# Kernel optimization log

Measured on AMD Instinct MI355X. Metric: run time of the kernel, lower is better.

The kernel has to match this reference:

```python
import jax, jax.numpy as jnp
import numpy as np

EPS = 1e-8


def setup_inputs() -> dict:
    key0 = jax.random.key(0)
    k1, k2, k3 = jax.random.split(key0, 3)
    B, Q, K, H, D = 8, 16, 65536, 1, 64
    query = jax.random.normal(k1, (B, Q, H, D), dtype=jnp.float32)
    key = jax.random.normal(k2, (B, K, H, D), dtype=jnp.float32)
    value = jax.random.normal(k3, (B, K, H, D), dtype=jnp.float32)
    return {"query": query, "key": key, "value": value}


def reference(query, key, value):
    # query: [B, Q, H, D]; key/value: [B, K, H, D]
    qk_features = query.shape[-1]
    q = query * (1.0 / np.sqrt(qk_features)).astype(np.float32)
    # scores: [B, H, Q, K]
    attn = jnp.einsum('bqhd,bkhd->bhqk', q, key)
    # inverted attention: softmax over the QUERY axis (-2)
    attn = jax.nn.softmax(attn, axis=-2)
    # renormalize over keys ('mean' norm_type)
    normalizer = jnp.sum(attn, axis=-1, keepdims=True) + EPS
    attn_n = attn / normalizer
    # updates: [B, Q, H, D]
    updates = jnp.einsum('bhqk,bkhd->bqhd', attn_n, value)
    # num_heads == 1 -> squeeze head dim: [B, Q, D]
    output = jnp.squeeze(updates, axis=-2)
    return (output, attn)
```

## Files before the change

### kernel.cpp

```cpp
#include <hip/hip_runtime.h>

#define KTOT 65536
#define QN 16
#define DN 64
#define BN 8
#define TILE 256

#define QS_OFF 0
#define R0_OFF 1024
#define R1_OFF 5120
#define SMEM_FLOATS 9216

__device__ __forceinline__ void gload_lds16(const float* g, float* l)
{
    __builtin_amdgcn_global_load_lds(
        (const __attribute__((address_space(1))) void*)g,
        (__attribute__((address_space(3))) void*)l, 16, 0, 0);
}

#define WAIT_VM(N)  do { asm volatile("s_waitcnt vmcnt(" #N ")" ::: "memory");      \
                         __builtin_amdgcn_sched_barrier(0); } while (0)
#define LGKM0()     do { asm volatile("s_waitcnt lgkmcnt(0)" ::: "memory");         \
                         __builtin_amdgcn_sched_barrier(0); } while (0)

#define STAGE_WV(RX, kb4, qo4)                                                      \
    {                                                                               \
        _Pragma("unroll")                                                           \
        for (int j = 0; j < 4; ++j) {                                               \
            const int r_ = (wv << 6) + (j << 4) + (lane >> 2);                      \
            const int p_ = (lane & 3) ^ ((r_ >> 1) & 3);                            \
            gload_lds16((const float*)((kb4) + r_ * 16 + (qo4) + p_),               \
                        (float*)(((float4*)&smem[RX]) + ((wv << 8) + (j << 6) + lane))); \
        }                                                                           \
    }

#define DOT_Q(qt, RX)                                                               \
    {                                                                               \
        _Pragma("unroll")                                                           \
        for (int cc = 0; cc < 4; ++cc) {                                            \
            const float4 kv = ((const float4*)&smem[RX])[tid * 4 + (cc ^ fr)];      \
            _Pragma("unroll")                                                       \
            for (int q = 0; q < QN; ++q) {                                          \
                const float4 qv = *reinterpret_cast<const float4*>(                 \
                    &smem[QS_OFF + q * DN + (qt) * 16 + cc * 4]);                   \
                s[q] = fmaf(kv.x, qv.x, s[q]);                                      \
                s[q] = fmaf(kv.y, qv.y, s[q]);                                      \
                s[q] = fmaf(kv.z, qv.z, s[q]);                                      \
                s[q] = fmaf(kv.w, qv.w, s[q]);                                      \
            }                                                                       \
        }                                                                           \
    }

__global__ __launch_bounds__(256, 3) void fused_attn(
    const float* __restrict__ query, const float* __restrict__ key,
    const float* __restrict__ value, float* __restrict__ attn,
    float* __restrict__ normp, float* __restrict__ upart,
    int NCH, int ntiles)
{
    __shared__ float smem[SMEM_FLOATS];
    const int b    = blockIdx.y;
    const int c    = blockIdx.x;
    const int tid  = threadIdx.x;
    const int wv   = tid >> 6;
    const int lane = tid & 63;
    const int chunk = ntiles * TILE;
    const int fr   = (tid >> 1) & 3;
    const int AW   = R1_OFF + wv * (QN * 64);

    {
        float4 qv = reinterpret_cast<const float4*>(query + (size_t)b * QN * DN)[tid];
        qv.x *= 0.125f; qv.y *= 0.125f; qv.z *= 0.125f; qv.w *= 0.125f;
        reinterpret_cast<float4*>(&smem[QS_OFF])[tid] = qv;
    }
    __syncthreads();

    {
        const float4* kb4 = reinterpret_cast<const float4*>(
            key + ((size_t)b * KTOT + c * chunk) * DN);
        STAGE_WV(R0_OFF, kb4, 0);
        STAGE_WV(R1_OFF, kb4, 4);
        __builtin_amdgcn_sched_barrier(0);
    }

    float U[QN], nacc[QN];
    #pragma unroll
    for (int q = 0; q < QN; ++q) { U[q] = 0.f; nacc[q] = 0.f; }

    for (int t = 0; t < ntiles; ++t) {
        const int krow0 = c * chunk + t * TILE;
        const float4* kb4  = reinterpret_cast<const float4*>(
            key + ((size_t)b * KTOT + krow0) * DN);
        const float4* kb4n = kb4 + TILE * 16;
        const float*  vptr = value + ((size_t)b * KTOT + krow0 + wv * 64) * DN + lane;

        float s[QN];
        #pragma unroll
        for (int q = 0; q < QN; ++q) s[q] = 0.f;

        WAIT_VM(4);
        DOT_Q(0, R0_OFF);
        LGKM0(); STAGE_WV(R0_OFF, kb4, 8);
        __builtin_amdgcn_sched_barrier(0);

        WAIT_VM(4);
        DOT_Q(1, R1_OFF);
        LGKM0(); STAGE_WV(R1_OFF, kb4, 12);
        __builtin_amdgcn_sched_barrier(0);

        WAIT_VM(4);
        DOT_Q(2, R0_OFF);

        float va[8];
        #pragma unroll
        for (int i = 0; i < 8; ++i) va[i] = vptr[(size_t)i * DN];
        __builtin_amdgcn_sched_barrier(0);
        WAIT_VM(8);
        DOT_Q(3, R1_OFF);

        float m = s[0];
        #pragma unroll
        for (int q = 1; q < QN; ++q) m = fmaxf(m, s[q]);
        float sum = 0.f;
        #pragma unroll
        for (int q = 0; q < QN; ++q) { s[q] = __expf(s[q] - m); sum += s[q]; }
        const float inv = 1.0f / sum;
        {
            float* ab = attn + (size_t)b * QN * KTOT + krow0 + tid;
            #pragma unroll
            for (int q = 0; q < QN; ++q) {
                const float a = s[q] * inv;
                __builtin_nontemporal_store(a, ab + (size_t)q * KTOT);
                smem[AW + q * 64 + lane] = a;
                nacc[q] += a;
            }
        }

        #pragma unroll 1
        for (int kk = 0; kk < 64; kk += 8) {
            float vb[8];
            const int nxt = kk + 8;
            if (nxt < 64) {
                #pragma unroll
                for (int i = 0; i < 8; ++i) vb[i] = vptr[(size_t)(nxt + i) * DN];
            }
            #pragma unroll
            for (int kq = 0; kq < 8; kq += 4) {
                #pragma unroll
                for (int q = 0; q < QN; ++q) {
                    const float4 av = *reinterpret_cast<const float4*>(
                        &smem[AW + q * 64 + kk + kq]);
                    U[q] = fmaf(av.x, va[kq + 0], U[q]);
                    U[q] = fmaf(av.y, va[kq + 1], U[q]);
                    U[q] = fmaf(av.z, va[kq + 2], U[q]);
                    U[q] = fmaf(av.w, va[kq + 3], U[q]);
                }
            }
            #pragma unroll
            for (int i = 0; i < 8; ++i) va[i] = vb[i];
        }

        if (t + 1 < ntiles) {
            LGKM0();
            STAGE_WV(R0_OFF, kb4n, 0);
            STAGE_WV(R1_OFF, kb4n, 4);
            __builtin_amdgcn_sched_barrier(0);
        }
    }

    __syncthreads();
    #pragma unroll
    for (int q = 0; q < QN; ++q)
        smem[R0_OFF + (wv * QN + q) * DN + lane] = U[q];
    #pragma unroll
    for (int q = 0; q < QN; ++q) {
        #pragma unroll
        for (int off = 1; off < 64; off <<= 1)
            nacc[q] += __shfl_xor(nacc[q], off, 64);
    }
    if (lane == 0) {
        #pragma unroll
        for (int q = 0; q < QN; ++q) smem[R1_OFF + wv * QN + q] = nacc[q];
    }
    __syncthreads();

    {
        const int q = tid >> 4, d0 = (tid & 15) * 4;
        const float4 r0 = *reinterpret_cast<const float4*>(&smem[R0_OFF + (0 * QN + q) * DN + d0]);
        const float4 r1 = *reinterpret_cast<const float4*>(&smem[R0_OFF + (1 * QN + q) * DN + d0]);
        const float4 r2 = *reinterpret_cast<const float4*>(&smem[R0_OFF + (2 * QN + q) * DN + d0]);
        const float4 r3 = *reinterpret_cast<const float4*>(&smem[R0_OFF + (3 * QN + q) * DN + d0]);
        float4 rs;
        rs.x = r0.x + r1.x + r2.x + r3.x;
        rs.y = r0.y + r1.y + r2.y + r3.y;
        rs.z = r0.z + r1.z + r2.z + r3.z;
        rs.w = r0.w + r1.w + r2.w + r3.w;
        *reinterpret_cast<float4*>(
            &upart[(((size_t)b * NCH + c) * QN + q) * DN + d0]) = rs;
        if (tid < QN)
            normp[((size_t)b * NCH + c) * QN + tid] =
                smem[R1_OFF + tid] + smem[R1_OFF + QN + tid] +
                smem[R1_OFF + 2 * QN + tid] + smem[R1_OFF + 3 * QN + tid];
    }
}

__global__ __launch_bounds__(256) void k3_fin(
    const float* __restrict__ upart, const float* __restrict__ normp,
    float* __restrict__ out, int NCH)
{
    const int b = blockIdx.x, q = blockIdx.y;
    const int tid = threadIdx.x;
    const int wv = tid >> 6, lane = tid & 63;

    float nv = 0.f;
    for (int c = tid; c < NCH; c += 256)
        nv += normp[((size_t)b * NCH + c) * QN + q];
    #pragma unroll
    for (int off = 1; off < 64; off <<= 1) nv += __shfl_xor(nv, off, 64);
    __shared__ float nred[4];
    if (lane == 0) nred[wv] = nv;

    float acc = 0.f;
    for (int c = wv; c < NCH; c += 4)
        acc += upart[(((size_t)b * NCH + c) * QN + q) * DN + lane];
    __shared__ float ured[4][DN];
    ured[wv][lane] = acc;
    __syncthreads();

    if (tid < DN) {
        const float n   = nred[0] + nred[1] + nred[2] + nred[3];
        const float inv = 1.0f / (n + 1e-8f);
        const float u   = ured[0][tid] + ured[1][tid] + ured[2][tid] + ured[3][tid];
        out[((size_t)b * QN + q) * DN + tid] = u * inv;
    }
}

extern "C" void kernel_launch(void* const* d_in, const int* in_sizes, int n_in,
                              void* d_out, int out_size, void* d_ws, size_t ws_size,
                              hipStream_t stream)
{
    const float* query = (const float*)d_in[0];
    const float* key   = (const float*)d_in[1];
    const float* value = (const float*)d_in[2];

    float* out  = (float*)d_out;
    float* attn = (float*)d_out + (size_t)BN * QN * DN;

    int NCH = 128;
    while (NCH > 8 && (size_t)BN * NCH * QN * (DN + 1) * 4 > ws_size) NCH >>= 1;
    const int ntiles = (KTOT / NCH) / TILE;

    float* normp = (float*)d_ws;
    float* upart = (float*)d_ws + (size_t)BN * NCH * QN;

    fused_attn<<<dim3(NCH, BN), 256, 0, stream>>>(query, key, value, attn,
                                                  normp, upart, NCH, ntiles);
    k3_fin   <<<dim3(BN, QN), 256, 0, stream>>>(upart, normp, out, NCH);
}
```

Before: 84.05 us.

## Compute key normalizer in finish kernel by rereading attn instead of accumulating

Drops the per-thread normalizer accumulators, their shuffle reduction and the normp workspace from the fused attention kernel. The finish kernel now sums each attn row directly from global memory. Occupancy bounds are raised from 3 to 4 blocks per CU, since fewer registers are needed. In exchange, the small finish grid must reread the whole 32 MB attention output.

```diff
diff --git a/kernel.cpp b/kernel.cpp
--- a/kernel.cpp
+++ b/kernel.cpp
@@ -51,11 +51,10 @@
         }                                                                           \
     }
 
-__global__ __launch_bounds__(256, 3) void fused_attn(
+__global__ __launch_bounds__(256, 4) void fused_attn(
     const float* __restrict__ query, const float* __restrict__ key,
     const float* __restrict__ value, float* __restrict__ attn,
-    float* __restrict__ normp, float* __restrict__ upart,
-    int NCH, int ntiles)
+    float* __restrict__ upart, int NCH, int ntiles)
 {
     __shared__ float smem[SMEM_FLOATS];
     const int b    = blockIdx.y;
@@ -82,9 +81,9 @@
         __builtin_amdgcn_sched_barrier(0);
     }
 
-    float U[QN], nacc[QN];
+    float U[QN];
     #pragma unroll
-    for (int q = 0; q < QN; ++q) { U[q] = 0.f; nacc[q] = 0.f; }
+    for (int q = 0; q < QN; ++q) U[q] = 0.f;
 
     for (int t = 0; t < ntiles; ++t) {
         const int krow0 = c * chunk + t * TILE;
@@ -131,7 +130,6 @@
                 const float a = s[q] * inv;
                 __builtin_nontemporal_store(a, ab + (size_t)q * KTOT);
                 smem[AW + q * 64 + lane] = a;
-                nacc[q] += a;
             }
         }
 
@@ -171,16 +169,6 @@
     #pragma unroll
     for (int q = 0; q < QN; ++q)
         smem[R0_OFF + (wv * QN + q) * DN + lane] = U[q];
-    #pragma unroll
-    for (int q = 0; q < QN; ++q) {
-        #pragma unroll
-        for (int off = 1; off < 64; off <<= 1)
-            nacc[q] += __shfl_xor(nacc[q], off, 64);
-    }
-    if (lane == 0) {
-        #pragma unroll
-        for (int q = 0; q < QN; ++q) smem[R1_OFF + wv * QN + q] = nacc[q];
-    }
     __syncthreads();
 
     {
@@ -196,24 +184,24 @@
         rs.w = r0.w + r1.w + r2.w + r3.w;
         *reinterpret_cast<float4*>(
             &upart[(((size_t)b * NCH + c) * QN + q) * DN + d0]) = rs;
-        if (tid < QN)
-            normp[((size_t)b * NCH + c) * QN + tid] =
-                smem[R1_OFF + tid] + smem[R1_OFF + QN + tid] +
-                smem[R1_OFF + 2 * QN + tid] + smem[R1_OFF + 3 * QN + tid];
     }
 }
 
 __global__ __launch_bounds__(256) void k3_fin(
-    const float* __restrict__ upart, const float* __restrict__ normp,
+    const float* __restrict__ attn, const float* __restrict__ upart,
     float* __restrict__ out, int NCH)
 {
     const int b = blockIdx.x, q = blockIdx.y;
     const int tid = threadIdx.x;
     const int wv = tid >> 6, lane = tid & 63;
 
+    const float4* ap = reinterpret_cast<const float4*>(attn + ((size_t)b * QN + q) * KTOT);
     float nv = 0.f;
-    for (int c = tid; c < NCH; c += 256)
-        nv += normp[((size_t)b * NCH + c) * QN + q];
+    #pragma unroll 4
+    for (int i = tid; i < KTOT / 4; i += 256) {
+        const float4 a = ap[i];
+        nv += (a.x + a.y) + (a.z + a.w);
+    }
     #pragma unroll
     for (int off = 1; off < 64; off <<= 1) nv += __shfl_xor(nv, off, 64);
     __shared__ float nred[4];
@@ -246,13 +234,12 @@
     float* attn = (float*)d_out + (size_t)BN * QN * DN;
 
     int NCH = 128;
-    while (NCH > 8 && (size_t)BN * NCH * QN * (DN + 1) * 4 > ws_size) NCH >>= 1;
+    while (NCH > 8 && (size_t)BN * NCH * QN * DN * 4 > ws_size) NCH >>= 1;
     const int ntiles = (KTOT / NCH) / TILE;
 
-    float* normp = (float*)d_ws;
-    float* upart = (float*)d_ws + (size_t)BN * NCH * QN;
+    float* upart = (float*)d_ws;
 
     fused_attn<<<dim3(NCH, BN), 256, 0, stream>>>(query, key, value, attn,
-                                                  normp, upart, NCH, ntiles);
-    k3_fin   <<<dim3(BN, QN), 256, 0, stream>>>(upart, normp, out, NCH);
-}
+                                                  upart, NCH, ntiles);
+    k3_fin   <<<dim3(BN, QN), 256, 0, stream>>>(attn, upart, out, NCH);
+}
```

Measured after the change: 83.36 us. About the same (-0.8%).
